# Performance work log

Measured on AMD Instinct MI355X. Metric: run time of the kernel, lower is better.

## Reference

```python
import jax, jax.numpy as jnp
import numpy as np

N, E, D, G, L, C, NI, NL = 100000, 1600000, 128, 1024, 3, 128, 100000, 64


def setup_inputs() -> dict:
    key = jax.random.key(0)
    ks = jax.random.split(key, 16)
    x = jax.random.normal(ks[0], (N, D), dtype=jnp.float32)
    src = jax.random.randint(ks[1], (E,), 0, N, dtype=jnp.int32)
    dst = jax.random.randint(ks[2], (E,), 0, N, dtype=jnp.int32)
    graph_ids = jnp.sort(jax.random.randint(ks[3], (N,), 0, G, dtype=jnp.int32))
    init_feat = jax.random.normal(ks[4], (NI, D), dtype=jnp.float32)
    init_graph_ids = jnp.sort(jax.random.randint(ks[5], (NI,), 0, G, dtype=jnp.int32))
    lead_feat = jax.random.normal(ks[6], (NL, D), dtype=jnp.float32)
    s = 1.0 / np.sqrt(D)
    W = jax.random.normal(ks[7], (L, D, D), dtype=jnp.float32) * s
    Wc = jax.random.normal(ks[8], (L, D, D), dtype=jnp.float32) * s
    b = jnp.zeros((L, D), dtype=jnp.float32)
    eps = jnp.zeros((L,), dtype=jnp.float32)
    fc1_w = jax.random.normal(ks[9], (D, D), dtype=jnp.float32) * s
    fc1_b = jnp.zeros((D,), dtype=jnp.float32)
    fc2_w = jax.random.normal(ks[10], (D, C), dtype=jnp.float32) * s
    fc2_b = jnp.zeros((C,), dtype=jnp.float32)
    return {"x": x, "src": src, "dst": dst, "graph_ids": graph_ids,
            "init_feat": init_feat, "init_graph_ids": init_graph_ids,
            "lead_feat": lead_feat, "W": W, "Wc": Wc, "b": b, "eps": eps,
            "fc1_w": fc1_w, "fc1_b": fc1_b, "fc2_w": fc2_w, "fc2_b": fc2_b,
            "num_graphs": G}


def reference(x, src, dst, graph_ids, init_feat, init_graph_ids, lead_feat,
              W, Wc, b, eps, fc1_w, fc1_b, fc2_w, fc2_b, num_graphs):
    n_nodes = x.shape[0]
    # global context: per-graph sum pooling of initial graph + lead graph sum
    h_init = jax.ops.segment_sum(init_feat, init_graph_ids, num_segments=num_graphs)  # [G,D]
    h_lead = jnp.sum(lead_feat, axis=0)  # [D]
    ctx = h_init[graph_ids] + h_lead  # [N,D], constant across layers

    h = x
    h_global = jax.ops.segment_sum(h, graph_ids, num_segments=num_graphs)  # [G,D]
    for l in range(W.shape[0]):
        agg = jax.ops.segment_sum(h[src], dst, num_segments=n_nodes)  # neighbor sum [N,D]
        m = (1.0 + eps[l]) * h + agg + h_global[graph_ids]
        h = jax.nn.relu(m @ W[l] + ctx @ Wc[l] + b[l])
        h_global = jax.ops.segment_sum(h, graph_ids, num_segments=num_graphs)
    out = jax.nn.relu(h_global @ fc1_w + fc1_b) @ fc2_w + fc2_b  # [G,C]
    return out
```

## Files before the change

### kernel.cpp

```cpp
#include <hip/hip_runtime.h>

#define D 128

typedef short short8_t __attribute__((ext_vector_type(8)));
typedef float float4_t __attribute__((ext_vector_type(4)));

#define BSH 8
#define BSZ 256
#define NBLK_A 256

__device__ __forceinline__ float bf_lo(unsigned u) { return __uint_as_float(u << 16); }
__device__ __forceinline__ float bf_hi(unsigned u) { return __uint_as_float(u & 0xffff0000u); }
__device__ __forceinline__ unsigned to_bf1(float x) {
    unsigned b = __float_as_uint(x);
    return (b + 0x7fffu + ((b >> 16) & 1u)) >> 16;
}
__device__ __forceinline__ unsigned pack2(float a, float b) {
    return to_bf1(a) | (to_bf1(b) << 16);
}


__global__ void f32_to_bf16(const float4* __restrict__ in, uint2* __restrict__ out, long n4) {
    long i = (long)blockIdx.x * blockDim.x + threadIdx.x;
    long stride = (long)gridDim.x * blockDim.x;
    for (; i < n4; i += stride) {
        float4 v = in[i];
        out[i] = make_uint2(pack2(v.x, v.y), pack2(v.z, v.w));
    }
}

__global__ void wpack(const float* __restrict__ W, uint4* __restrict__ Wpk, int L_) {
    int id = blockIdx.x * blockDim.x + threadIdx.x;
    if (id >= L_ * 2048) return;
    int lane = id & 63, cc = (id >> 6) & 3, t = (id >> 8) & 7, l = id >> 11;
    int n = t * 16 + (lane & 15);
    int k0 = cc * 32 + (lane >> 4) * 8;
    const float* Wb = W + (long)l * D * D;
    unsigned u0 = pack2(Wb[(long)(k0 + 0) * D + n], Wb[(long)(k0 + 1) * D + n]);
    unsigned u1 = pack2(Wb[(long)(k0 + 2) * D + n], Wb[(long)(k0 + 3) * D + n]);
    unsigned u2 = pack2(Wb[(long)(k0 + 4) * D + n], Wb[(long)(k0 + 5) * D + n]);
    unsigned u3 = pack2(Wb[(long)(k0 + 6) * D + n], Wb[(long)(k0 + 7) * D + n]);
    Wpk[id] = make_uint4(u0, u1, u2, u3);
}


__global__ __launch_bounds__(256)
void csr_hist(const int* __restrict__ dst, int* __restrict__ Hist, int E_, int chunk) {
    __shared__ int h[512];
    int b = blockIdx.x, t = threadIdx.x;
    h[t] = 0; h[t + 256] = 0;
    __syncthreads();
    int base = b * chunk;
    int end = base + chunk; if (end > E_) end = E_;
    for (int i = base + t; i < end; i += 256)
        atomicAdd(&h[dst[i] >> BSH], 1);
    __syncthreads();
    Hist[b * 512 + t] = h[t];
    Hist[b * 512 + t + 256] = h[t + 256];
}

__global__ __launch_bounds__(256)
void csr_scan_blocks(int* __restrict__ Hist, int* __restrict__ Tot) {
    __shared__ int sc[256];
    int bkt = blockIdx.x, t = threadIdx.x;
    int v = Hist[t * 512 + bkt];
    sc[t] = v; __syncthreads();
    for (int off = 1; off < 256; off <<= 1) {
        int u = (t >= off) ? sc[t - off] : 0;
        __syncthreads();
        sc[t] += u;
        __syncthreads();
    }
    Hist[t * 512 + bkt] = sc[t] - v;
    if (t == 255) Tot[bkt] = sc[255];
}

__global__ __launch_bounds__(512)
void csr_scan_base(const int* __restrict__ Tot, int* __restrict__ Base, int NB) {
    __shared__ int sc[512];
    int t = threadIdx.x;
    int v = (t < NB) ? Tot[t] : 0;
    sc[t] = v; __syncthreads();
    for (int off = 1; off < 512; off <<= 1) {
        int u = (t >= off) ? sc[t - off] : 0;
        __syncthreads();
        sc[t] += u;
        __syncthreads();
    }
    Base[t] = sc[t] - v;
    if (t == NB - 1) Base[NB] = sc[t];
}

__global__ __launch_bounds__(256)
void csr_scatter(const int* __restrict__ src, const int* __restrict__ dst,
                 const int* __restrict__ Hist, const int* __restrict__ Base,
                 unsigned* __restrict__ EdgeBuf, int E_, int chunk) {
    __shared__ int cur[512];
    int b = blockIdx.x, t = threadIdx.x;
    cur[t]       = Base[t]       + Hist[b * 512 + t];
    cur[t + 256] = Base[t + 256] + Hist[b * 512 + t + 256];
    __syncthreads();
    int base = b * chunk;
    int end = base + chunk; if (end > E_) end = E_;
    for (int i = base + t; i < end; i += 256) {
        int s = src[i], dd = dst[i];
        int p = atomicAdd(&cur[dd >> BSH], 1);
        EdgeBuf[p] = (unsigned)s | ((unsigned)(dd & (BSZ - 1)) << 24);
    }
}

__global__ __launch_bounds__(256)
void csr_fill(const unsigned* __restrict__ EdgeBuf, const int* __restrict__ Base,
              int* __restrict__ rowptr, int* __restrict__ csr, int N_, int E_) {
    __shared__ int deg[256];
    __shared__ int cur[256];
    int b = blockIdx.x, t = threadIdx.x;
    int e0 = Base[b], e1 = Base[b + 1];
    deg[t] = 0;
    __syncthreads();
    for (int i = e0 + t; i < e1; i += 256)
        atomicAdd(&deg[EdgeBuf[i] >> 24], 1);
    __syncthreads();
    int v = deg[t];
    cur[t] = v; __syncthreads();
    for (int off = 1; off < 256; off <<= 1) {
        int u = (t >= off) ? cur[t - off] : 0;
        __syncthreads();
        cur[t] += u;
        __syncthreads();
    }
    int excl = cur[t] - v;
    int node = b * BSZ + t;
    if (node < N_) rowptr[node] = e0 + excl;
    cur[t] = e0 + excl;
    __syncthreads();
    for (int i = e0 + t; i < e1; i += 256) {
        unsigned ev = EdgeBuf[i];
        int p = atomicAdd(&cur[ev >> 24], 1);
        csr[p] = (int)(ev & 0x00FFFFFFu);
    }
    if (b == 0 && t == 0) rowptr[N_] = E_;
}

__global__ void find_starts(const int* __restrict__ gids, int n, int G_,
                            int* __restrict__ start) {
    int g = blockIdx.x * blockDim.x + threadIdx.x;
    if (g > G_) return;
    if (g == G_) { start[g] = n; return; }
    int lo = 0, hi = n;
    while (lo < hi) { int mid = (lo + hi) >> 1; if (gids[mid] < g) lo = mid + 1; else hi = mid; }
    start[g] = lo;
}


__global__ void reduce_lead(const float* __restrict__ lead, float* __restrict__ hlead, int NL) {
    int d = threadIdx.x;
    float a0 = 0.f, a1 = 0.f, a2 = 0.f, a3 = 0.f;
    int r = 0;
    for (; r + 4 <= NL; r += 4) {
        a0 += lead[(long)r * D + d];
        a1 += lead[(long)(r + 1) * D + d];
        a2 += lead[(long)(r + 2) * D + d];
        a3 += lead[(long)(r + 3) * D + d];
    }
    for (; r < NL; ++r) a0 += lead[(long)r * D + d];
    hlead[d] = a0 + a1 + a2 + a3;
}

__global__ __launch_bounds__(128)
void segsum_pg(const float* __restrict__ feat, const int* __restrict__ start,
               const float* __restrict__ addv, float* __restrict__ out) {
    int g = blockIdx.x;
    int d = threadIdx.x;
    int r0 = start[g], r1 = start[g + 1];
    float a0 = 0.f, a1 = 0.f, a2 = 0.f, a3 = 0.f;
    int r = r0;
    for (; r + 4 <= r1; r += 4) {
        a0 += feat[(long)r * D + d];
        a1 += feat[(long)(r + 1) * D + d];
        a2 += feat[(long)(r + 2) * D + d];
        a3 += feat[(long)(r + 3) * D + d];
    }
    for (; r < r1; ++r) a0 += feat[(long)r * D + d];
    float s = a0 + a1 + a2 + a3;
    if (addv) s += addv[d];
    out[(long)g * D + d] = s;
}

__global__ __launch_bounds__(128)
void graph_term(const unsigned* __restrict__ hb, const int* __restrict__ start,
                const float* __restrict__ ctx, const float* __restrict__ Wl,
                const float* __restrict__ Wcl, const float* __restrict__ bl,
                float* __restrict__ T) {
    __shared__ float xs[D];
    __shared__ float cs[D];
    int g = blockIdx.x, tid = threadIdx.x;
    int r0 = start[g], r1 = start[g + 1];
    int c = tid >> 1;
    bool hi = tid & 1;
    float a0=0,a1=0,a2=0,a3=0,a4=0,a5=0,a6=0,a7=0;
    int r = r0;
    for (; r + 8 <= r1; r += 8) {
        unsigned u0 = hb[(long)(r+0)*64+c], u1 = hb[(long)(r+1)*64+c];
        unsigned u2 = hb[(long)(r+2)*64+c], u3 = hb[(long)(r+3)*64+c];
        unsigned u4 = hb[(long)(r+4)*64+c], u5 = hb[(long)(r+5)*64+c];
        unsigned u6 = hb[(long)(r+6)*64+c], u7 = hb[(long)(r+7)*64+c];
        a0 += hi ? bf_hi(u0) : bf_lo(u0);
        a1 += hi ? bf_hi(u1) : bf_lo(u1);
        a2 += hi ? bf_hi(u2) : bf_lo(u2);
        a3 += hi ? bf_hi(u3) : bf_lo(u3);
        a4 += hi ? bf_hi(u4) : bf_lo(u4);
        a5 += hi ? bf_hi(u5) : bf_lo(u5);
        a6 += hi ? bf_hi(u6) : bf_lo(u6);
        a7 += hi ? bf_hi(u7) : bf_lo(u7);
    }
    for (; r < r1; ++r) {
        unsigned u = hb[(long)r*64+c];
        a0 += hi ? bf_hi(u) : bf_lo(u);
    }
    xs[tid] = ((a0+a1)+(a2+a3)) + ((a4+a5)+(a6+a7));
    cs[tid] = ctx[(long)g * D + tid];
    __syncthreads();
    float p0=0,p1=0,p2=0,p3=0;
    for (int k = 0; k < D; k += 4) {
        p0 += xs[k]   * Wl[(long)k*D + tid];
        p1 += xs[k+1] * Wl[(long)(k+1)*D + tid];
        p2 += xs[k+2] * Wl[(long)(k+2)*D + tid];
        p3 += xs[k+3] * Wl[(long)(k+3)*D + tid];
    }
    for (int k = 0; k < D; k += 4) {
        p0 += cs[k]   * Wcl[(long)k*D + tid];
        p1 += cs[k+1] * Wcl[(long)(k+1)*D + tid];
        p2 += cs[k+2] * Wcl[(long)(k+2)*D + tid];
        p3 += cs[k+3] * Wcl[(long)(k+3)*D + tid];
    }
    T[(long)g * D + tid] = bl[tid] + (p0 + p1) + (p2 + p3);
}

__global__ __launch_bounds__(128)
void readout(const unsigned* __restrict__ hb, const int* __restrict__ start,
             const float* __restrict__ f1w, const float* __restrict__ f1b,
             const float* __restrict__ f2w, const float* __restrict__ f2b,
             float* __restrict__ out) {
    __shared__ float xs[D];
    __shared__ float zs[D];
    int g = blockIdx.x, tid = threadIdx.x;
    int r0 = start[g], r1 = start[g + 1];
    int c = tid >> 1;
    bool hi = tid & 1;
    float a0=0,a1=0,a2=0,a3=0;
    int r = r0;
    for (; r + 4 <= r1; r += 4) {
        unsigned u0 = hb[(long)(r+0)*64+c], u1 = hb[(long)(r+1)*64+c];
        unsigned u2 = hb[(long)(r+2)*64+c], u3 = hb[(long)(r+3)*64+c];
        a0 += hi ? bf_hi(u0) : bf_lo(u0);
        a1 += hi ? bf_hi(u1) : bf_lo(u1);
        a2 += hi ? bf_hi(u2) : bf_lo(u2);
        a3 += hi ? bf_hi(u3) : bf_lo(u3);
    }
    for (; r < r1; ++r) {
        unsigned u = hb[(long)r*64+c];
        a0 += hi ? bf_hi(u) : bf_lo(u);
    }
    xs[tid] = (a0+a1)+(a2+a3);
    __syncthreads();
    float p0=0,p1=0,p2=0,p3=0;
    for (int k = 0; k < D; k += 4) {
        p0 += xs[k]   * f1w[(long)k*D + tid];
        p1 += xs[k+1] * f1w[(long)(k+1)*D + tid];
        p2 += xs[k+2] * f1w[(long)(k+2)*D + tid];
        p3 += xs[k+3] * f1w[(long)(k+3)*D + tid];
    }
    zs[tid] = fmaxf(f1b[tid] + (p0+p1)+(p2+p3), 0.f);
    __syncthreads();
    float q0=0,q1=0,q2=0,q3=0;
    for (int k = 0; k < D; k += 4) {
        q0 += zs[k]   * f2w[(long)k*D + tid];
        q1 += zs[k+1] * f2w[(long)(k+1)*D + tid];
        q2 += zs[k+2] * f2w[(long)(k+2)*D + tid];
        q3 += zs[k+3] * f2w[(long)(k+3)*D + tid];
    }
    out[(long)g * D + tid] = f2b[tid] + (q0+q1)+(q2+q3);
}

#define TROWS 64
__global__ __launch_bounds__(256, 6)
void layer_kernel(const unsigned* __restrict__ hb, const uint4* __restrict__ Wpk_l,
                  const float* __restrict__ T, const int* __restrict__ gids,
                  const int* __restrict__ rowptr, const int* __restrict__ csr,
                  const float* __restrict__ eps_l, unsigned* __restrict__ houtb, int n) {
    __shared__ __align__(16) unsigned Minb[TROWS][68];
    int tid = threadIdx.x;
    int w = tid >> 6, lane = tid & 63;
    int w16 = w * 16;
    int rowBase = blockIdx.x * TROWS;
    int rb = rowBase + w16;
    float epsv = 1.0f + *eps_l;

    int rp = rb + lane; if (rp > n) rp = n;
    int evv = rowptr[rp];

    int e0 = __shfl(evv, 0);
    int e1 = __shfl(evv, 1);
    int idxv = (e0 + lane < e1) ? csr[e0 + lane] : 0;

    for (int i = 0; i < 16; ++i) {
        int r = rb + i;
        int deg = e1 - e0;
        int e0n = __shfl(evv, i + 1);
        int e1n = __shfl(evv, i + 2);
        int idxn = (e0n + lane < e1n) ? csr[e0n + lane] : 0;
        float sx = 0.f, sy = 0.f;
        if (r < n) {
            unsigned su = hb[(long)r * 64 + lane];
            float ax0 = epsv * bf_lo(su), ay0 = epsv * bf_hi(su);
            float ax1=0,ay1=0,ax2=0,ay2=0,ax3=0,ay3=0;
            int iv = idxv;
            int base = 0;
            while (true) {
                int m = deg - base; if (m > 64) m = 64;
                int j = 0;
                for (; j + 8 <= m; j += 8) {
                    int s0=__shfl(iv,j+0), s1=__shfl(iv,j+1), s2=__shfl(iv,j+2), s3=__shfl(iv,j+3);
                    int s4=__shfl(iv,j+4), s5=__shfl(iv,j+5), s6=__shfl(iv,j+6), s7=__shfl(iv,j+7);
                    unsigned u0=hb[(long)s0*64+lane], u1=hb[(long)s1*64+lane];
                    unsigned u2=hb[(long)s2*64+lane], u3=hb[(long)s3*64+lane];
                    unsigned u4=hb[(long)s4*64+lane], u5=hb[(long)s5*64+lane];
                    unsigned u6=hb[(long)s6*64+lane], u7=hb[(long)s7*64+lane];
                    ax0+=bf_lo(u0); ay0+=bf_hi(u0); ax1+=bf_lo(u1); ay1+=bf_hi(u1);
                    ax2+=bf_lo(u2); ay2+=bf_hi(u2); ax3+=bf_lo(u3); ay3+=bf_hi(u3);
                    ax0+=bf_lo(u4); ay0+=bf_hi(u4); ax1+=bf_lo(u5); ay1+=bf_hi(u5);
                    ax2+=bf_lo(u6); ay2+=bf_hi(u6); ax3+=bf_lo(u7); ay3+=bf_hi(u7);
                }
                for (; j < m; ++j) {
                    int s = __shfl(iv, j);
                    unsigned u = hb[(long)s * 64 + lane];
                    ax0 += bf_lo(u); ay0 += bf_hi(u);
                }
                base += 64;
                if (base >= deg) break;
                int mm = deg - base;
                iv = (lane < mm) ? csr[e0 + base + lane] : 0;
            }
            sx = (ax0 + ax1) + (ax2 + ax3);
            sy = (ay0 + ay1) + (ay2 + ay3);
        }
        Minb[w16 + i][lane] = pack2(sx, sy);
        e0 = e0n; e1 = e1n; idxv = idxn;
    }

    int m_ = lane & 15, quad = lane >> 4;
    float4_t acc[8];
    #pragma unroll
    for (int tt = 0; tt < 8; ++tt) { acc[tt][0]=0.f; acc[tt][1]=0.f; acc[tt][2]=0.f; acc[tt][3]=0.f; }

    #pragma unroll
    for (int cc = 0; cc < 4; ++cc) {
        short8_t af = *(const short8_t*)&Minb[w16 + m_][cc * 16 + quad * 4];
        #pragma unroll
        for (int tt = 0; tt < 8; ++tt) {
            short8_t bf = *(const short8_t*)&Wpk_l[(tt * 4 + cc) * 64 + lane];
            acc[tt] = __builtin_amdgcn_mfma_f32_16x16x32_bf16(af, bf, acc[tt], 0, 0, 0);
        }
    }

    int gq[4];
    #pragma unroll
    for (int reg = 0; reg < 4; ++reg) {
        int r = rb + quad * 4 + reg;
        gq[reg] = (r < n) ? gids[r] : 0;
    }
    #pragma unroll
    for (int tt = 0; tt < 8; ++tt) {
        int col = tt * 16 + m_;
        #pragma unroll
        for (int reg = 0; reg < 4; ++reg) {
            float v = acc[tt][reg] + T[(long)gq[reg] * D + col];
            v = fmaxf(v, 0.f);
            float v2 = __shfl_xor(v, 1);
            if (!(lane & 1)) Minb[w16 + quad * 4 + reg][tt * 8 + (m_ >> 1)] = pack2(v, v2);
        }
    }
    #pragma unroll
    for (int rr = 0; rr < 4; ++rr) {
        int lrow = rr * 4 + (lane >> 4);
        int r = rowBase + w16 + lrow;
        if (r < n) {
            uint4 v = *(const uint4*)&Minb[w16 + lrow][(lane & 15) * 4];
            *(uint4*)&houtb[(long)r * 64 + (lane & 15) * 4] = v;
        }
    }
}


static inline size_t align512(size_t x) { return (x + 511) & ~(size_t)511; }

extern "C" void kernel_launch(void* const* d_in, const int* in_sizes, int n_in,
                              void* d_out, int out_size, void* d_ws, size_t ws_size,
                              hipStream_t stream) {
    const float* x        = (const float*)d_in[0];
    const int*   src      = (const int*)d_in[1];
    const int*   dst      = (const int*)d_in[2];
    const int*   gids     = (const int*)d_in[3];
    const float* initf    = (const float*)d_in[4];
    const int*   init_gid = (const int*)d_in[5];
    const float* leadf    = (const float*)d_in[6];
    const float* W        = (const float*)d_in[7];
    const float* Wc       = (const float*)d_in[8];
    const float* b        = (const float*)d_in[9];
    const float* eps      = (const float*)d_in[10];
    const float* fc1_w    = (const float*)d_in[11];
    const float* fc1_b    = (const float*)d_in[12];
    const float* fc2_w    = (const float*)d_in[13];
    const float* fc2_b    = (const float*)d_in[14];
    float* out = (float*)d_out;

    const int N  = in_sizes[0] / D;
    const int E  = in_sizes[1];
    const int NL = in_sizes[6] / D;
    const int L  = in_sizes[10];

    char* p = (char*)d_ws;
    unsigned* xb  = (unsigned*)p; p += align512((size_t)N * 64 * 4);
    unsigned* hAb = (unsigned*)p; p += align512((size_t)N * 64 * 4);
    unsigned* hBb = (unsigned*)p; p += align512((size_t)N * 64 * 4);
    const int G = 1024;
    float* T     = (float*)p; p += align512((size_t)G * D * 4);
    float* ctx   = (float*)p; p += align512((size_t)G * D * 4);
    float* hlead = (float*)p; p += align512((size_t)D * 4);
    int* rowptr  = (int*)p;   p += align512((size_t)(N + 1) * 4);
    int* csr     = (int*)p;   p += align512((size_t)E * 4);
    unsigned* EdgeBuf = (unsigned*)p; p += align512((size_t)E * 4);
    int* Hist    = (int*)p;   p += align512((size_t)NBLK_A * 512 * 4);
    int* Tot     = (int*)p;   p += align512((size_t)520 * 4);
    int* Base    = (int*)p;   p += align512((size_t)520 * 4);
    int* nstart  = (int*)p;   p += align512((size_t)(G + 1) * 4);
    int* istart  = (int*)p;   p += align512((size_t)(G + 1) * 4);
    uint4* Wpk   = (uint4*)p; p += align512((size_t)L * 2048 * 16);
    (void)ws_size; (void)n_in;

    const int NB = (N + BSZ - 1) / BSZ;
    const int chunk = (E + NBLK_A - 1) / NBLK_A;

    csr_hist<<<NBLK_A, 256, 0, stream>>>(dst, Hist, E, chunk);
    csr_scan_blocks<<<NB, 256, 0, stream>>>(Hist, Tot);
    csr_scan_base<<<1, 512, 0, stream>>>(Tot, Base, NB);
    csr_scatter<<<NBLK_A, 256, 0, stream>>>(src, dst, Hist, Base, EdgeBuf, E, chunk);
    csr_fill<<<NB, 256, 0, stream>>>(EdgeBuf, Base, rowptr, csr, N, E);

    f32_to_bf16<<<2048, 256, 0, stream>>>((const float4*)x, (uint2*)xb, (long)N * D / 4);
    wpack<<<(L * 2048 + 255) / 256, 256, 0, stream>>>(W, Wpk, L);

    find_starts<<<(G + 256) / 256, 256, 0, stream>>>(gids, N, G, nstart);
    find_starts<<<(G + 256) / 256, 256, 0, stream>>>(init_gid, in_sizes[4] / D, G, istart);

    reduce_lead<<<1, D, 0, stream>>>(leadf, hlead, NL);
    segsum_pg<<<G, D, 0, stream>>>(initf, istart, hlead, ctx);

    const unsigned* hcur = xb;
    unsigned* bufs[2] = { hAb, hBb };
    int layerBlocks = (N + TROWS - 1) / TROWS;
    for (int l = 0; l < L; ++l) {
        graph_term<<<G, D, 0, stream>>>(hcur, nstart, ctx, W + (long)l * D * D,
                                        Wc + (long)l * D * D, b + (long)l * D, T);
        unsigned* hnext = bufs[l & 1];
        layer_kernel<<<layerBlocks, 256, 0, stream>>>(hcur, Wpk + (size_t)l * 2048, T,
                                                      gids, rowptr, csr,
                                                      eps + l, hnext, N);
        hcur = hnext;
    }

    readout<<<G, D, 0, stream>>>(hcur, nstart, fc1_w, fc1_b, fc2_w, fc2_b, out);
}
```

Before: 534.9 us.

## Precompute ctx@Wc per layer, widen gather loads, shrink layer blocks

The context projection ctx@Wc+b is now computed once for all layers in a new ctx_prep kernel, which also folds in the lead-feature reduction. The per-layer graph kernel therefore only reduces h and multiplies by W. Neighbor gathers in layer_kernel now have each half-wave fetch a different neighbor with 8-byte loads, and the halves are combined with a cross-half shuffle. The block size drops to 128 threads with 32 rows per block. The epilogue also skips per-row graph-id loads when a 16-row tile belongs to a single graph, and the two find_starts launches are merged into one. This adds launch-config and register-pressure changes whose net effect on occupancy is unclear.

```diff
diff --git a/kernel.cpp b/kernel.cpp
--- a/kernel.cpp
+++ b/kernel.cpp
@@ -142,99 +142,89 @@
     if (b == 0 && t == 0) rowptr[N_] = E_;
 }
 
-__global__ void find_starts(const int* __restrict__ gids, int n, int G_,
-                            int* __restrict__ start) {
-    int g = blockIdx.x * blockDim.x + threadIdx.x;
-    if (g > G_) return;
-    if (g == G_) { start[g] = n; return; }
+__global__ void find_starts2(const int* __restrict__ g1, int n1,
+                             const int* __restrict__ g2, int n2,
+                             int G_, int* __restrict__ s1, int* __restrict__ s2) {
+    int id = blockIdx.x * blockDim.x + threadIdx.x;
+    if (id >= 2 * (G_ + 1)) return;
+    const int* arr; int n; int* out; int g;
+    if (id <= G_) { arr = g1; n = n1; out = s1; g = id; }
+    else { arr = g2; n = n2; out = s2; g = id - (G_ + 1); }
+    if (g == G_) { out[g] = n; return; }
     int lo = 0, hi = n;
-    while (lo < hi) { int mid = (lo + hi) >> 1; if (gids[mid] < g) lo = mid + 1; else hi = mid; }
-    start[g] = lo;
-}
-
-
-__global__ void reduce_lead(const float* __restrict__ lead, float* __restrict__ hlead, int NL) {
-    int d = threadIdx.x;
-    float a0 = 0.f, a1 = 0.f, a2 = 0.f, a3 = 0.f;
-    int r = 0;
-    for (; r + 4 <= NL; r += 4) {
-        a0 += lead[(long)r * D + d];
-        a1 += lead[(long)(r + 1) * D + d];
-        a2 += lead[(long)(r + 2) * D + d];
-        a3 += lead[(long)(r + 3) * D + d];
-    }
-    for (; r < NL; ++r) a0 += lead[(long)r * D + d];
-    hlead[d] = a0 + a1 + a2 + a3;
+    while (lo < hi) { int mid = (lo + hi) >> 1; if (arr[mid] < g) lo = mid + 1; else hi = mid; }
+    out[g] = lo;
 }
 
 __global__ __launch_bounds__(128)
-void segsum_pg(const float* __restrict__ feat, const int* __restrict__ start,
-               const float* __restrict__ addv, float* __restrict__ out) {
-    int g = blockIdx.x;
-    int d = threadIdx.x;
-    int r0 = start[g], r1 = start[g + 1];
+void ctx_prep(const float* __restrict__ initf, const int* __restrict__ istart,
+              const float* __restrict__ leadf, int NL,
+              const float* __restrict__ Wc, const float* __restrict__ bb, int L_,
+              float* __restrict__ ctxT) {
+    __shared__ float cs[D];
+    int g = blockIdx.x, t = threadIdx.x;
+    float hl = 0.f;
+    for (int r = 0; r < NL; ++r) hl += leadf[(long)r * D + t];
+    int r0 = istart[g], r1 = istart[g + 1];
     float a0 = 0.f, a1 = 0.f, a2 = 0.f, a3 = 0.f;
     int r = r0;
     for (; r + 4 <= r1; r += 4) {
-        a0 += feat[(long)r * D + d];
-        a1 += feat[(long)(r + 1) * D + d];
-        a2 += feat[(long)(r + 2) * D + d];
-        a3 += feat[(long)(r + 3) * D + d];
-    }
-    for (; r < r1; ++r) a0 += feat[(long)r * D + d];
-    float s = a0 + a1 + a2 + a3;
-    if (addv) s += addv[d];
-    out[(long)g * D + d] = s;
+        a0 += initf[(long)r * D + t];
+        a1 += initf[(long)(r + 1) * D + t];
+        a2 += initf[(long)(r + 2) * D + t];
+        a3 += initf[(long)(r + 3) * D + t];
+    }
+    for (; r < r1; ++r) a0 += initf[(long)r * D + t];
+    cs[t] = hl + (a0 + a1) + (a2 + a3);
+    __syncthreads();
+    for (int l = 0; l < L_; ++l) {
+        const float* Wcl = Wc + (long)l * D * D;
+        float p0 = 0.f, p1 = 0.f, p2 = 0.f, p3 = 0.f;
+        for (int k = 0; k < D; k += 4) {
+            p0 += cs[k]     * Wcl[(long)k * D + t];
+            p1 += cs[k + 1] * Wcl[(long)(k + 1) * D + t];
+            p2 += cs[k + 2] * Wcl[(long)(k + 2) * D + t];
+            p3 += cs[k + 3] * Wcl[(long)(k + 3) * D + t];
+        }
+        ctxT[((long)l * gridDim.x + g) * D + t] = bb[l * D + t] + (p0 + p1) + (p2 + p3);
+    }
 }
 
 __global__ __launch_bounds__(128)
-void graph_term(const unsigned* __restrict__ hb, const int* __restrict__ start,
-                const float* __restrict__ ctx, const float* __restrict__ Wl,
-                const float* __restrict__ Wcl, const float* __restrict__ bl,
-                float* __restrict__ T) {
+void segsum_T(const unsigned* __restrict__ hb, const int* __restrict__ start,
+              const float* __restrict__ Wl, const float* __restrict__ ctxT_l,
+              float* __restrict__ T) {
+    __shared__ float part[2][64][2];
     __shared__ float xs[D];
-    __shared__ float cs[D];
-    int g = blockIdx.x, tid = threadIdx.x;
+    int g = blockIdx.x, t = threadIdx.x;
+    int c = t & 63, half = t >> 6;
     int r0 = start[g], r1 = start[g + 1];
-    int c = tid >> 1;
-    bool hi = tid & 1;
-    float a0=0,a1=0,a2=0,a3=0,a4=0,a5=0,a6=0,a7=0;
-    int r = r0;
-    for (; r + 8 <= r1; r += 8) {
-        unsigned u0 = hb[(long)(r+0)*64+c], u1 = hb[(long)(r+1)*64+c];
-        unsigned u2 = hb[(long)(r+2)*64+c], u3 = hb[(long)(r+3)*64+c];
-        unsigned u4 = hb[(long)(r+4)*64+c], u5 = hb[(long)(r+5)*64+c];
-        unsigned u6 = hb[(long)(r+6)*64+c], u7 = hb[(long)(r+7)*64+c];
-        a0 += hi ? bf_hi(u0) : bf_lo(u0);
-        a1 += hi ? bf_hi(u1) : bf_lo(u1);
-        a2 += hi ? bf_hi(u2) : bf_lo(u2);
-        a3 += hi ? bf_hi(u3) : bf_lo(u3);
-        a4 += hi ? bf_hi(u4) : bf_lo(u4);
-        a5 += hi ? bf_hi(u5) : bf_lo(u5);
-        a6 += hi ? bf_hi(u6) : bf_lo(u6);
-        a7 += hi ? bf_hi(u7) : bf_lo(u7);
-    }
-    for (; r < r1; ++r) {
-        unsigned u = hb[(long)r*64+c];
-        a0 += hi ? bf_hi(u) : bf_lo(u);
-    }
-    xs[tid] = ((a0+a1)+(a2+a3)) + ((a4+a5)+(a6+a7));
-    cs[tid] = ctx[(long)g * D + tid];
+    float l0=0,h0=0,l1=0,h1=0,l2=0,h2=0,l3=0,h3=0;
+    int r = r0 + half;
+    for (; r + 6 < r1; r += 8) {
+        unsigned a = hb[(long)r * 64 + c];
+        unsigned bq = hb[(long)(r + 2) * 64 + c];
+        unsigned cq = hb[(long)(r + 4) * 64 + c];
+        unsigned dq = hb[(long)(r + 6) * 64 + c];
+        l0 += bf_lo(a);  h0 += bf_hi(a);
+        l1 += bf_lo(bq); h1 += bf_hi(bq);
+        l2 += bf_lo(cq); h2 += bf_hi(cq);
+        l3 += bf_lo(dq); h3 += bf_hi(dq);
+    }
+    for (; r < r1; r += 2) { unsigned a = hb[(long)r * 64 + c]; l0 += bf_lo(a); h0 += bf_hi(a); }
+    part[half][c][0] = (l0 + l1) + (l2 + l3);
+    part[half][c][1] = (h0 + h1) + (h2 + h3);
+    __syncthreads();
+    xs[t] = part[0][t >> 1][t & 1] + part[1][t >> 1][t & 1];
     __syncthreads();
     float p0=0,p1=0,p2=0,p3=0;
     for (int k = 0; k < D; k += 4) {
-        p0 += xs[k]   * Wl[(long)k*D + tid];
-        p1 += xs[k+1] * Wl[(long)(k+1)*D + tid];
-        p2 += xs[k+2] * Wl[(long)(k+2)*D + tid];
-        p3 += xs[k+3] * Wl[(long)(k+3)*D + tid];
-    }
-    for (int k = 0; k < D; k += 4) {
-        p0 += cs[k]   * Wcl[(long)k*D + tid];
-        p1 += cs[k+1] * Wcl[(long)(k+1)*D + tid];
-        p2 += cs[k+2] * Wcl[(long)(k+2)*D + tid];
-        p3 += cs[k+3] * Wcl[(long)(k+3)*D + tid];
-    }
-    T[(long)g * D + tid] = bl[tid] + (p0 + p1) + (p2 + p3);
+        p0 += xs[k]     * Wl[(long)k * D + t];
+        p1 += xs[k + 1] * Wl[(long)(k + 1) * D + t];
+        p2 += xs[k + 2] * Wl[(long)(k + 2) * D + t];
+        p3 += xs[k + 3] * Wl[(long)(k + 3) * D + t];
+    }
+    T[(long)g * D + t] = ctxT_l[(long)g * D + t] + (p0 + p1) + (p2 + p3);
 }
 
 __global__ __launch_bounds__(128)
@@ -242,49 +232,47 @@
              const float* __restrict__ f1w, const float* __restrict__ f1b,
              const float* __restrict__ f2w, const float* __restrict__ f2b,
              float* __restrict__ out) {
+    __shared__ float part[2][64][2];
     __shared__ float xs[D];
     __shared__ float zs[D];
-    int g = blockIdx.x, tid = threadIdx.x;
+    int g = blockIdx.x, t = threadIdx.x;
+    int c = t & 63, half = t >> 6;
     int r0 = start[g], r1 = start[g + 1];
-    int c = tid >> 1;
-    bool hi = tid & 1;
-    float a0=0,a1=0,a2=0,a3=0;
-    int r = r0;
-    for (; r + 4 <= r1; r += 4) {
-        unsigned u0 = hb[(long)(r+0)*64+c], u1 = hb[(long)(r+1)*64+c];
-        unsigned u2 = hb[(long)(r+2)*64+c], u3 = hb[(long)(r+3)*64+c];
-        a0 += hi ? bf_hi(u0) : bf_lo(u0);
-        a1 += hi ? bf_hi(u1) : bf_lo(u1);
-        a2 += hi ? bf_hi(u2) : bf_lo(u2);
-        a3 += hi ? bf_hi(u3) : bf_lo(u3);
-    }
-    for (; r < r1; ++r) {
-        unsigned u = hb[(long)r*64+c];
-        a0 += hi ? bf_hi(u) : bf_lo(u);
-    }
-    xs[tid] = (a0+a1)+(a2+a3);
+    float l0=0,h0=0,l1=0,h1=0;
+    int r = r0 + half;
+    for (; r + 2 < r1; r += 4) {
+        unsigned a = hb[(long)r * 64 + c];
+        unsigned bq = hb[(long)(r + 2) * 64 + c];
+        l0 += bf_lo(a);  h0 += bf_hi(a);
+        l1 += bf_lo(bq); h1 += bf_hi(bq);
+    }
+    if (r < r1) { unsigned a = hb[(long)r * 64 + c]; l0 += bf_lo(a); h0 += bf_hi(a); }
+    part[half][c][0] = l0 + l1;
+    part[half][c][1] = h0 + h1;
+    __syncthreads();
+    xs[t] = part[0][t >> 1][t & 1] + part[1][t >> 1][t & 1];
     __syncthreads();
     float p0=0,p1=0,p2=0,p3=0;
     for (int k = 0; k < D; k += 4) {
-        p0 += xs[k]   * f1w[(long)k*D + tid];
-        p1 += xs[k+1] * f1w[(long)(k+1)*D + tid];
-        p2 += xs[k+2] * f1w[(long)(k+2)*D + tid];
-        p3 += xs[k+3] * f1w[(long)(k+3)*D + tid];
-    }
-    zs[tid] = fmaxf(f1b[tid] + (p0+p1)+(p2+p3), 0.f);
+        p0 += xs[k]     * f1w[(long)k * D + t];
+        p1 += xs[k + 1] * f1w[(long)(k + 1) * D + t];
+        p2 += xs[k + 2] * f1w[(long)(k + 2) * D + t];
+        p3 += xs[k + 3] * f1w[(long)(k + 3) * D + t];
+    }
+    zs[t] = fmaxf(f1b[t] + (p0 + p1) + (p2 + p3), 0.f);
     __syncthreads();
     float q0=0,q1=0,q2=0,q3=0;
     for (int k = 0; k < D; k += 4) {
-        q0 += zs[k]   * f2w[(long)k*D + tid];
-        q1 += zs[k+1] * f2w[(long)(k+1)*D + tid];
-        q2 += zs[k+2] * f2w[(long)(k+2)*D + tid];
-        q3 += zs[k+3] * f2w[(long)(k+3)*D + tid];
-    }
-    out[(long)g * D + tid] = f2b[tid] + (q0+q1)+(q2+q3);
-}
-
-#define TROWS 64
-__global__ __launch_bounds__(256, 6)
+        q0 += zs[k]     * f2w[(long)k * D + t];
+        q1 += zs[k + 1] * f2w[(long)(k + 1) * D + t];
+        q2 += zs[k + 2] * f2w[(long)(k + 2) * D + t];
+        q3 += zs[k + 3] * f2w[(long)(k + 3) * D + t];
+    }
+    out[(long)g * D + t] = f2b[t] + (q0 + q1) + (q2 + q3);
+}
+
+#define TROWS 32
+__global__ __launch_bounds__(128, 6)
 void layer_kernel(const unsigned* __restrict__ hb, const uint4* __restrict__ Wpk_l,
                   const float* __restrict__ T, const int* __restrict__ gids,
                   const int* __restrict__ rowptr, const int* __restrict__ csr,
@@ -292,6 +280,7 @@
     __shared__ __align__(16) unsigned Minb[TROWS][68];
     int tid = threadIdx.x;
     int w = tid >> 6, lane = tid & 63;
+    int pl = lane & 31;
     int w16 = w * 16;
     int rowBase = blockIdx.x * TROWS;
     int rb = rowBase + w16;
@@ -310,42 +299,57 @@
         int e0n = __shfl(evv, i + 1);
         int e1n = __shfl(evv, i + 2);
         int idxn = (e0n + lane < e1n) ? csr[e0n + lane] : 0;
-        float sx = 0.f, sy = 0.f;
+        unsigned su = (r < n) ? hb[(long)r * 64 + lane] : 0u;
+        float ax0=0, ay0=0, ax1=0, ay1=0;
+        float bx0=0, by0=0, bx1=0, by1=0;
         if (r < n) {
-            unsigned su = hb[(long)r * 64 + lane];
-            float ax0 = epsv * bf_lo(su), ay0 = epsv * bf_hi(su);
-            float ax1=0,ay1=0,ax2=0,ay2=0,ax3=0,ay3=0;
             int iv = idxv;
             int base = 0;
             while (true) {
                 int m = deg - base; if (m > 64) m = 64;
                 int j = 0;
-                for (; j + 8 <= m; j += 8) {
-                    int s0=__shfl(iv,j+0), s1=__shfl(iv,j+1), s2=__shfl(iv,j+2), s3=__shfl(iv,j+3);
-                    int s4=__shfl(iv,j+4), s5=__shfl(iv,j+5), s6=__shfl(iv,j+6), s7=__shfl(iv,j+7);
-                    unsigned u0=hb[(long)s0*64+lane], u1=hb[(long)s1*64+lane];
-                    unsigned u2=hb[(long)s2*64+lane], u3=hb[(long)s3*64+lane];
-                    unsigned u4=hb[(long)s4*64+lane], u5=hb[(long)s5*64+lane];
-                    unsigned u6=hb[(long)s6*64+lane], u7=hb[(long)s7*64+lane];
-                    ax0+=bf_lo(u0); ay0+=bf_hi(u0); ax1+=bf_lo(u1); ay1+=bf_hi(u1);
-                    ax2+=bf_lo(u2); ay2+=bf_hi(u2); ax3+=bf_lo(u3); ay3+=bf_hi(u3);
-                    ax0+=bf_lo(u4); ay0+=bf_hi(u4); ax1+=bf_lo(u5); ay1+=bf_hi(u5);
-                    ax2+=bf_lo(u6); ay2+=bf_hi(u6); ax3+=bf_lo(u7); ay3+=bf_hi(u7);
+                for (; j + 4 <= m; j += 4) {
+                    int sa0 = __shfl(iv, j+0), sa1 = __shfl(iv, j+1);
+                    int sb0 = __shfl(iv, j+2), sb1 = __shfl(iv, j+3);
+                    int sA = (lane & 32) ? sa1 : sa0;
+                    int sB = (lane & 32) ? sb1 : sb0;
+                    uint2 uA = *(const uint2*)(hb + (long)sA * 64 + pl * 2);
+                    uint2 uB = *(const uint2*)(hb + (long)sB * 64 + pl * 2);
+                    ax0 += bf_lo(uA.x); ay0 += bf_hi(uA.x);
+                    ax1 += bf_lo(uA.y); ay1 += bf_hi(uA.y);
+                    bx0 += bf_lo(uB.x); by0 += bf_hi(uB.x);
+                    bx1 += bf_lo(uB.y); by1 += bf_hi(uB.y);
                 }
-                for (; j < m; ++j) {
+                for (; j + 2 <= m; j += 2) {
+                    int sa0 = __shfl(iv, j), sa1 = __shfl(iv, j+1);
+                    int sA = (lane & 32) ? sa1 : sa0;
+                    uint2 uA = *(const uint2*)(hb + (long)sA * 64 + pl * 2);
+                    ax0 += bf_lo(uA.x); ay0 += bf_hi(uA.x);
+                    ax1 += bf_lo(uA.y); ay1 += bf_hi(uA.y);
+                }
+                if (j < m) {
                     int s = __shfl(iv, j);
-                    unsigned u = hb[(long)s * 64 + lane];
-                    ax0 += bf_lo(u); ay0 += bf_hi(u);
+                    if (!(lane & 32)) {
+                        uint2 u = *(const uint2*)(hb + (long)s * 64 + pl * 2);
+                        ax0 += bf_lo(u.x); ay0 += bf_hi(u.x);
+                        ax1 += bf_lo(u.y); ay1 += bf_hi(u.y);
+                    }
                 }
                 base += 64;
                 if (base >= deg) break;
                 int mm = deg - base;
                 iv = (lane < mm) ? csr[e0 + base + lane] : 0;
             }
-            sx = (ax0 + ax1) + (ax2 + ax3);
-            sy = (ay0 + ay1) + (ay2 + ay3);
-        }
-        Minb[w16 + i][lane] = pack2(sx, sy);
+        }
+        float s0 = ax0 + bx0, s1 = ay0 + by0, s2 = ax1 + bx1, s3 = ay1 + by1;
+        s0 += __shfl_xor(s0, 32); s1 += __shfl_xor(s1, 32);
+        s2 += __shfl_xor(s2, 32); s3 += __shfl_xor(s3, 32);
+        unsigned ue = __shfl(su, 2 * pl);
+        unsigned uo = __shfl(su, 2 * pl + 1);
+        s0 += epsv * bf_lo(ue); s1 += epsv * bf_hi(ue);
+        s2 += epsv * bf_lo(uo); s3 += epsv * bf_hi(uo);
+        if (!(lane & 32))
+            *(uint2*)&Minb[w16 + i][2 * pl] = make_uint2(pack2(s0, s1), pack2(s2, s3));
         e0 = e0n; e1 = e1n; idxv = idxn;
     }
 
@@ -364,21 +368,47 @@
         }
     }
 
+    int g0 = 0; bool uni = false;
+    if (rb < n) {
+        int lastr = rb + 15 < n ? rb + 15 : n - 1;
+        g0 = gids[rb];
+        uni = (g0 == gids[lastr]);
+    }
     int gq[4];
-    #pragma unroll
-    for (int reg = 0; reg < 4; ++reg) {
-        int r = rb + quad * 4 + reg;
-        gq[reg] = (r < n) ? gids[r] : 0;
+    if (!uni) {
+        #pragma unroll
+        for (int reg = 0; reg < 4; ++reg) {
+            int r = rb + quad * 4 + reg;
+            gq[reg] = (r < n) ? gids[r] : 0;
+        }
     }
     #pragma unroll
     for (int tt = 0; tt < 8; ++tt) {
         int col = tt * 16 + m_;
-        #pragma unroll
-        for (int reg = 0; reg < 4; ++reg) {
-            float v = acc[tt][reg] + T[(long)gq[reg] * D + col];
-            v = fmaxf(v, 0.f);
-            float v2 = __shfl_xor(v, 1);
-            if (!(lane & 1)) Minb[w16 + quad * 4 + reg][tt * 8 + (m_ >> 1)] = pack2(v, v2);
+        float t0, t1, t2, t3;
+        if (uni) {
+            float tv = T[(long)g0 * D + col];
+            t0 = t1 = t2 = t3 = tv;
+        } else {
+            t0 = T[(long)gq[0] * D + col];
+            t1 = T[(long)gq[1] * D + col];
+            t2 = T[(long)gq[2] * D + col];
+            t3 = T[(long)gq[3] * D + col];
+        }
+        float v0 = fmaxf(acc[tt][0] + t0, 0.f);
+        float v1 = fmaxf(acc[tt][1] + t1, 0.f);
+        float v2 = fmaxf(acc[tt][2] + t2, 0.f);
+        float v3 = fmaxf(acc[tt][3] + t3, 0.f);
+        float w0 = __shfl_xor(v0, 1);
+        float w1 = __shfl_xor(v1, 1);
+        float w2 = __shfl_xor(v2, 1);
+        float w3 = __shfl_xor(v3, 1);
+        if (!(lane & 1)) {
+            int cu = tt * 8 + (m_ >> 1);
+            Minb[w16 + quad * 4 + 0][cu] = pack2(v0, w0);
+            Minb[w16 + quad * 4 + 1][cu] = pack2(v1, w1);
+            Minb[w16 + quad * 4 + 2][cu] = pack2(v2, w2);
+            Minb[w16 + quad * 4 + 3][cu] = pack2(v3, w3);
         }
     }
     #pragma unroll
@@ -417,6 +447,7 @@
 
     const int N  = in_sizes[0] / D;
     const int E  = in_sizes[1];
+    const int NI = in_sizes[4] / D;
     const int NL = in_sizes[6] / D;
     const int L  = in_sizes[10];
 
@@ -426,8 +457,7 @@
     unsigned* hBb = (unsigned*)p; p += align512((size_t)N * 64 * 4);
     const int G = 1024;
     float* T     = (float*)p; p += align512((size_t)G * D * 4);
-    float* ctx   = (float*)p; p += align512((size_t)G * D * 4);
-    float* hlead = (float*)p; p += align512((size_t)D * 4);
+    float* ctxT  = (float*)p; p += align512((size_t)L * G * D * 4);
     int* rowptr  = (int*)p;   p += align512((size_t)(N + 1) * 4);
     int* csr     = (int*)p;   p += align512((size_t)E * 4);
     unsigned* EdgeBuf = (unsigned*)p; p += align512((size_t)E * 4);
@@ -450,21 +480,19 @@
 
     f32_to_bf16<<<2048, 256, 0, stream>>>((const float4*)x, (uint2*)xb, (long)N * D / 4);
     wpack<<<(L * 2048 + 255) / 256, 256, 0, stream>>>(W, Wpk, L);
-
-    find_starts<<<(G + 256) / 256, 256, 0, stream>>>(gids, N, G, nstart);
-    find_starts<<<(G + 256) / 256, 256, 0, stream>>>(init_gid, in_sizes[4] / D, G, istart);
-
-    reduce_lead<<<1, D, 0, stream>>>(leadf, hlead, NL);
-    segsum_pg<<<G, D, 0, stream>>>(initf, istart, hlead, ctx);
+    find_starts2<<<(2 * (G + 1) + 255) / 256, 256, 0, stream>>>(gids, N, init_gid, NI,
+                                                                G, nstart, istart);
+
+    ctx_prep<<<G, D, 0, stream>>>(initf, istart, leadf, NL, Wc, b, L, ctxT);
 
     const unsigned* hcur = xb;
     unsigned* bufs[2] = { hAb, hBb };
     int layerBlocks = (N + TROWS - 1) / TROWS;
     for (int l = 0; l < L; ++l) {
-        graph_term<<<G, D, 0, stream>>>(hcur, nstart, ctx, W + (long)l * D * D,
-                                        Wc + (long)l * D * D, b + (long)l * D, T);
+        segsum_T<<<G, D, 0, stream>>>(hcur, nstart, W + (long)l * D * D,
+                                      ctxT + (long)l * G * D, T);
         unsigned* hnext = bufs[l & 1];
-        layer_kernel<<<layerBlocks, 256, 0, stream>>>(hcur, Wpk + (size_t)l * 2048, T,
+        layer_kernel<<<layerBlocks, 128, 0, stream>>>(hcur, Wpk + (size_t)l * 2048, T,
                                                       gids, rowptr, csr,
                                                       eps + l, hnext, N);
         hcur = hnext;
```

Measured after the change: 697.7 us. 1.3x slower.
